# Optimization experiments

Measured on AMD Instinct MI355X. Metric: run time of the kernel, lower is better.

Reference implementation:

```python
import jax, jax.numpy as jnp
import numpy as np

MAX_SEGMENTS = 256
MAX_PIXELS = 400   # fixed-capacity bucket per segment
EMBED_DIM = 768
N_CHANNELS = 3


def setup_inputs() -> dict:
    key = jax.random.key(0)
    k1, k2, k3, k4 = jax.random.split(key, 4)
    img = jax.random.normal(k1, (32, N_CHANNELS, 384, 384), dtype=jnp.float32)
    segments = jax.random.randint(k2, (32, 384, 384), 0, MAX_SEGMENTS, dtype=jnp.int32)
    fan_in = N_CHANNELS * MAX_PIXELS
    proj_w = jax.random.normal(k3, (EMBED_DIM, fan_in), dtype=jnp.float32) / np.sqrt(fan_in).astype(np.float32)
    proj_b = jax.random.normal(k4, (EMBED_DIM,), dtype=jnp.float32) * 0.01
    return {"img": img, "segments": segments, "proj_w": proj_w, "proj_b": proj_b}


def _bucketize(img_flat, seg_flat):
    """img_flat: [C, N] pixels in row-major scan order; seg_flat: [N] int ids.
    Returns [S, C*P]: first P pixels (scan order) of each segment, zero padded,
    channel-major per segment — matching torch's masked gather + flatten."""
    C, N = img_flat.shape
    idx = jnp.arange(N, dtype=jnp.int32)
    # stable sort by segment id preserves scan order within each segment
    order = jnp.argsort(seg_flat, stable=True)
    sorted_seg = seg_flat[order]
    is_start = jnp.concatenate([jnp.ones((1,), bool), sorted_seg[1:] != sorted_seg[:-1]])
    group_start = jax.lax.cummax(jnp.where(is_start, idx, 0))
    rank_sorted = idx - group_start                      # position within segment
    rank = jnp.zeros((N,), jnp.int32).at[order].set(rank_sorted)
    dump = MAX_SEGMENTS * MAX_PIXELS                      # overflow slot (discarded)
    dest = jnp.where(rank < MAX_PIXELS, seg_flat.astype(jnp.int32) * MAX_PIXELS + rank, dump)
    buf = jnp.zeros((C, dump + 1), img_flat.dtype).at[:, dest].set(img_flat)
    # [C, S, P] -> [S, C, P] -> [S, C*P] (channel-major flatten per segment)
    return buf[:, :dump].reshape(C, MAX_SEGMENTS, MAX_PIXELS).transpose(1, 0, 2).reshape(MAX_SEGMENTS, C * MAX_PIXELS)


def reference(img, segments, proj_w, proj_b):
    B, C, H, W = img.shape
    feats = jax.vmap(_bucketize)(img.reshape(B, C, H * W), segments.reshape(B, H * W))
    # [B, S, C*P] @ [C*P, E] + [E]
    return feats @ proj_w.T + proj_b
```

## Files before the change

kernel.cpp:

```cpp
#include <hip/hip_runtime.h>
#include <hip/hip_bf16.h>
#include <cstdint>

#define BATCH 32
#define NCH 3
#define HW 147456
#define NSEG 256
#define NPIX 400
#define KDIM 1200
#define EDIM 768
#define MROWS (BATCH * NSEG)

#define CHUNK 4096
#define NCHUNK (HW / CHUNK)
#define NW 8
#define SUBW (CHUNK / NW)

#define ROW_BYTES 4800
#define APK_BYTES ((size_t)MROWS * ROW_BYTES)
#define W_BYTES (EDIM * KDIM * 4)

typedef __attribute__((ext_vector_type(8))) short short8b;
typedef __attribute__((ext_vector_type(16))) float f32x16;

__device__ __forceinline__ uint32_t bf16_rn(float f) {
    uint32_t u = __float_as_uint(f);
    return (u + 0x7fffu + ((u >> 16) & 1u)) >> 16;
}
__device__ __forceinline__ float bf16_tof(uint32_t h) { return __uint_as_float(h << 16); }
__device__ __forceinline__ uint32_t pack_split(float v) {
    uint32_t hi = bf16_rn(v);
    uint32_t lo = bf16_rn(v - bf16_tof(hi));
    return (lo << 16) | hi;
}

__device__ __forceinline__ void async_copy16(const void* gsrc, void* ldst) {
    __builtin_amdgcn_global_load_lds(
        (const __attribute__((address_space(1))) uint32_t*)gsrc,
        (__attribute__((address_space(3))) uint32_t*)ldst, 16, 0, 0);
}

__global__ __launch_bounds__(256) void hist_kernel(const int* __restrict__ seg,
                                                   int* __restrict__ cnt) {
    __shared__ int h[NSEG];
    const int tid = threadIdx.x;
    h[tid] = 0;
    __syncthreads();
    const int blk = blockIdx.x;
    const int b = blk / NCHUNK, ck = blk % NCHUNK;
    const int* segb = seg + (size_t)b * HW + ck * CHUNK;
#pragma unroll
    for (int i = 0; i < CHUNK / 256; ++i) atomicAdd(&h[segb[i * 256 + tid]], 1);
    __syncthreads();
    cnt[blk * NSEG + tid] = h[tid];
}

__global__ __launch_bounds__(256) void scan_kernel(int* __restrict__ cnt) {
    const int t = blockIdx.x * 256 + threadIdx.x;
    const int b = t >> 8, s = t & 255;
    int run = 0;
#pragma unroll
    for (int ck = 0; ck < NCHUNK; ++ck) {
        int* p = cnt + ((size_t)(b * NCHUNK + ck)) * NSEG + s;
        int v = *p;
        *p = run;
        run += v;
    }
    cnt[(size_t)(b * NCHUNK) * NSEG + s] = run;
}

__global__ __launch_bounds__(512) void scatter_kernel(const float* __restrict__ img,
                                                      const int* __restrict__ seg,
                                                      const int* __restrict__ base,
                                                      uint8_t* __restrict__ apk) {
    __shared__ int wpos[NW][NSEG];
    __shared__ int sl[NSEG];
    __shared__ uint32_t st0[CHUNK], st1[CHUNK], st2[CHUNK];

    const int tid = threadIdx.x;
    const int lane = tid & 63;
    const int wid = tid >> 6;
    const int blk = blockIdx.x;
    const int b = blk / NCHUNK, ck = blk % NCHUNK;

    int sb = 0;
    if (tid < NSEG) sb = (ck == 0) ? 0 : base[(size_t)blk * NSEG + tid];
#pragma unroll
    for (int i = 0; i < (NW * NSEG) / 512; ++i) ((int*)wpos)[i * 512 + tid] = 0;
    __syncthreads();

    const int* segb = seg + (size_t)b * HW;
    const float* imgb = img + (size_t)b * NCH * HW;
    const int startp = ck * CHUNK + wid * SUBW;
    const unsigned long long lt = (lane == 0) ? 0ull : ((~0ull) >> (64 - lane));

    int sv[SUBW / 64];
    unsigned long long mv[SUBW / 64];
#pragma unroll
    for (int g = 0; g < SUBW / 64; ++g) {
        const int p = startp + g * 64 + lane;
        const int s = segb[p];
        unsigned long long m = ~0ull;
#pragma unroll
        for (int bit = 0; bit < 8; ++bit) {
            unsigned long long bal = __ballot((s >> bit) & 1);
            m &= ((s >> bit) & 1) ? bal : ~bal;
        }
        sv[g] = s; mv[g] = m;
        if ((m & lt) == 0ull) atomicAdd(&wpos[wid][s], __popcll(m));
    }
    __syncthreads();

    int csum = 0;
    if (tid < NSEG) {
        int r = sb;
#pragma unroll
        for (int w = 0; w < NW; ++w) {
            const int t = wpos[w][tid];
            wpos[w][tid] = r;
            r += t;
        }
        csum = r - sb;
        sl[tid] = csum;
    }
    __syncthreads();
#pragma unroll
    for (int off = 1; off < NSEG; off <<= 1) {
        int y = 0;
        if (tid < NSEG && tid >= off) y = sl[tid - off];
        __syncthreads();
        if (tid < NSEG) sl[tid] += y;
        __syncthreads();
    }
    {
        int excl = 0;
        if (tid < NSEG) excl = sl[tid] - csum;
        __syncthreads();
        if (tid < NSEG) sl[tid] = (sb << 13) | excl;
    }
    __syncthreads();

#pragma unroll
    for (int g = 0; g < SUBW / 64; ++g) {
        const int p = startp + g * 64 + lane;
        const int s = sv[g];
        const unsigned long long m = mv[g];
        const int rig = __popcll(m & lt);
        const int leader = __ffsll((unsigned long long)m) - 1;
        int old = 0;
        if (rig == 0) old = atomicAdd(&wpos[wid][s], __popcll(m));
        old = __shfl(old, leader, 64);
        const int rank = old + rig;
        const int v = sl[s];
        const int j = rank - (v >> 13) + (v & 8191);
        st0[j] = pack_split(imgb[p]);
        st1[j] = pack_split(imgb[HW + p]);
        st2[j] = pack_split(imgb[2 * HW + p]);
    }
    __syncthreads();

    uint8_t* apkb = apk + (size_t)b * NSEG * ROW_BYTES;
#pragma unroll
    for (int it = 0; it < CHUNK / 512; ++it) {
        const int j = it * 512 + tid;
        int s = 0;
#pragma unroll
        for (int step = 128; step; step >>= 1) {
            const int c = s + step;
            if (c < NSEG && (sl[c] & 8191) <= j) s = c;
        }
        const int v = sl[s];
        const int rank = (v >> 13) + (j - (v & 8191));
        if (rank < NPIX) {
            uint16_t* hp = (uint16_t*)(apkb + (size_t)s * ROW_BYTES);
            uint16_t* lp = (uint16_t*)(apkb + (size_t)s * ROW_BYTES + 2400);
            const uint32_t v0 = st0[j], v1 = st1[j], v2 = st2[j];
            hp[rank]       = (uint16_t)v0;  lp[rank]       = (uint16_t)(v0 >> 16);
            hp[400 + rank] = (uint16_t)v1;  lp[400 + rank] = (uint16_t)(v1 >> 16);
            hp[800 + rank] = (uint16_t)v2;  lp[800 + rank] = (uint16_t)(v2 >> 16);
        }
    }
}

__global__ __launch_bounds__(256) void tailzero_kernel(uint8_t* __restrict__ apk,
                                                       const int* __restrict__ cnt) {
    const int tid = threadIdx.x;
    const int l = tid & 63;
    const int wid = tid >> 6;
    const int row = blockIdx.x * 4 + wid;
    const int b = row >> 8, s = row & 255;
    const int tot = cnt[(size_t)(b * NCHUNK) * NSEG + s];
    if (tot >= NPIX) return;
    uint16_t* hp = (uint16_t*)(apk + (size_t)row * ROW_BYTES);
    uint16_t* lp = (uint16_t*)(apk + (size_t)row * ROW_BYTES + 2400);
    for (int r = tot + l; r < NPIX; r += 64) {
        hp[r] = 0; lp[r] = 0;
        hp[400 + r] = 0; lp[400 + r] = 0;
        hp[800 + r] = 0; lp[800 + r] = 0;
    }
}

__global__ __launch_bounds__(256) void repackW_kernel(float* __restrict__ w) {
    __shared__ float buf[4][KDIM];
    const int tid = threadIdx.x;
    const int l = tid & 63;
    const int wid = tid >> 6;
    const int row = blockIdx.x * 4 + wid;
    float* rowp = w + (size_t)row * KDIM;
#pragma unroll
    for (int i = 0; i < 19; ++i) {
        const int idx = i * 64 + l;
        if (idx < KDIM) buf[wid][idx] = rowp[idx];
    }
    __syncthreads();
    uint32_t* rowu = (uint32_t*)rowp;
#pragma unroll
    for (int i = 0; i < 10; ++i) {
        const int j = i * 64 + l;
        if (j < KDIM / 2) {
            const float f0 = buf[wid][2 * j], f1 = buf[wid][2 * j + 1];
            const uint32_t h0 = bf16_rn(f0), h1 = bf16_rn(f1);
            const uint32_t l0 = bf16_rn(f0 - bf16_tof(h0));
            const uint32_t l1 = bf16_rn(f1 - bf16_tof(h1));
            rowu[j]            = h0 | (h1 << 16);
            rowu[KDIM / 2 + j] = l0 | (l1 << 16);
        }
    }
}

__global__ __launch_bounds__(256) void gemm_kernel(const uint8_t* __restrict__ A,
                                                   const uint8_t* __restrict__ Wp,
                                                   const float* __restrict__ bias,
                                                   float* __restrict__ out) {
    __shared__ uint8_t smem[49152];

    const int tid = threadIdx.x;
    const int l = tid & 63;
    const int wid = tid >> 6;
    const int wm = wid >> 1, wn = wid & 1;

    const int bid = blockIdx.x;
    const int xcd = bid & 7;
    const int t = bid >> 3;
    const int bn = t % 12;
    const int bm = (t / 12) * 8 + xcd;

    const int swzl = ((l & 7) * 16) ^ ((l >> 3) << 4);
    const int xread = (l & 7) << 4;

    const uint8_t* Abase = A + (size_t)bm * 128 * ROW_BYTES;

    f32x16 acc[2] = {};

    for (int k0 = 0; k0 < KDIM; k0 += 64) {
#pragma unroll
        for (int ii = 0; ii < 4; ++ii) {
            const int i = wid * 4 + ii;
            const int row = i * 8 + (l >> 3);
            const size_t gb = (size_t)row * ROW_BYTES + k0 * 2 + swzl;
            async_copy16(Abase + gb,        smem + i * 1024);
            async_copy16(Abase + gb + 2400, smem + 16384 + i * 1024);
        }
#pragma unroll
        for (int ii = 0; ii < 2; ++ii) {
            const int i = wid * 2 + ii;
            const int row = i * 8 + (l >> 3);
            const size_t gb = (size_t)(bn * 64 + row) * ROW_BYTES + k0 * 2 + swzl;
            async_copy16(Wp + gb, smem + 32768 + i * 1024);
            size_t gl = gb + 2400;
            if (gl + 16 > (size_t)W_BYTES) gl = 0;
            async_copy16(Wp + gl, smem + 40960 + i * 1024);
        }
        __syncthreads();

#pragma unroll
        for (int ks = 0; ks < 4; ++ks) {
            if (k0 + ks * 16 >= KDIM) break;
            const int koff = ks * 32 + ((l >> 5) * 16);
            short8b ahi[2], alo[2], bhi, blo;
#pragma unroll
            for (int mi = 0; mi < 2; ++mi) {
                const int row = wm * 64 + mi * 32 + (l & 31);
                const int byteA = row * 128 + (koff ^ xread);
                ahi[mi] = *(const short8b*)(smem + byteA);
                alo[mi] = *(const short8b*)(smem + 16384 + byteA);
            }
            {
                const int row = wn * 32 + (l & 31);
                const int byteB = row * 128 + (koff ^ xread);
                bhi = *(const short8b*)(smem + 32768 + byteB);
                blo = *(const short8b*)(smem + 40960 + byteB);
            }
#pragma unroll
            for (int mi = 0; mi < 2; ++mi) {
                acc[mi] = __builtin_amdgcn_mfma_f32_32x32x16_bf16(ahi[mi], bhi, acc[mi], 0, 0, 0);
                acc[mi] = __builtin_amdgcn_mfma_f32_32x32x16_bf16(ahi[mi], blo, acc[mi], 0, 0, 0);
                acc[mi] = __builtin_amdgcn_mfma_f32_32x32x16_bf16(alo[mi], bhi, acc[mi], 0, 0, 0);
            }
        }
        __syncthreads();
    }

    const int e = bn * 64 + wn * 32 + (l & 31);
    const float bv = bias[e];
#pragma unroll
    for (int mi = 0; mi < 2; ++mi) {
        const int rbase = bm * 128 + wm * 64 + mi * 32 + 4 * (l >> 5);
#pragma unroll
        for (int r = 0; r < 16; ++r) {
            const int row = rbase + (r & 3) + 8 * (r >> 2);
            out[(size_t)row * EDIM + e] = acc[mi][r] + bv;
        }
    }
}

extern "C" void kernel_launch(void* const* d_in, const int* in_sizes, int n_in,
                              void* d_out, int out_size, void* d_ws, size_t ws_size,
                              hipStream_t stream) {
    const float* img      = (const float*)d_in[0];
    const int*   segments = (const int*)d_in[1];
    float*       proj_w   = (float*)d_in[2];
    const float* proj_b   = (const float*)d_in[3];
    float* out = (float*)d_out;

    uint8_t* apk = (uint8_t*)d_ws;
    int*     cnt = (int*)((char*)d_ws + APK_BYTES);

    hist_kernel<<<BATCH * NCHUNK, 256, 0, stream>>>(segments, cnt);
    scan_kernel<<<MROWS / 256, 256, 0, stream>>>(cnt);
    repackW_kernel<<<EDIM / 4, 256, 0, stream>>>(proj_w);
    scatter_kernel<<<BATCH * NCHUNK, 512, 0, stream>>>(img, segments, cnt, apk);
    tailzero_kernel<<<MROWS / 4, 256, 0, stream>>>(apk, cnt);

    gemm_kernel<<<64 * 12, 256, 0, stream>>>(apk, (const uint8_t*)proj_w, proj_b, out);
}
```

Measured before the change: 224.8 us.

## Widen scatter blocks to 1024 threads, use wave-shuffle scan and segment map

```diff
diff --git a/kernel.cpp b/kernel.cpp
--- a/kernel.cpp
+++ b/kernel.cpp
@@ -13,7 +13,7 @@
 
 #define CHUNK 4096
 #define NCHUNK (HW / CHUNK)
-#define NW 8
+#define NW 16
 #define SUBW (CHUNK / NW)
 
 #define ROW_BYTES 4800
@@ -58,23 +58,26 @@
 __global__ __launch_bounds__(256) void scan_kernel(int* __restrict__ cnt) {
     const int t = blockIdx.x * 256 + threadIdx.x;
     const int b = t >> 8, s = t & 255;
+    int* basep = cnt + (size_t)(b * NCHUNK) * NSEG + s;
+    int v[NCHUNK];
+#pragma unroll
+    for (int ck = 0; ck < NCHUNK; ++ck) v[ck] = basep[ck * NSEG];
     int run = 0;
 #pragma unroll
-    for (int ck = 0; ck < NCHUNK; ++ck) {
-        int* p = cnt + ((size_t)(b * NCHUNK + ck)) * NSEG + s;
-        int v = *p;
-        *p = run;
-        run += v;
-    }
-    cnt[(size_t)(b * NCHUNK) * NSEG + s] = run;
-}
-
-__global__ __launch_bounds__(512) void scatter_kernel(const float* __restrict__ img,
-                                                      const int* __restrict__ seg,
-                                                      const int* __restrict__ base,
-                                                      uint8_t* __restrict__ apk) {
+    for (int ck = 0; ck < NCHUNK; ++ck) { const int x = v[ck]; v[ck] = run; run += x; }
+    v[0] = run;
+#pragma unroll
+    for (int ck = 0; ck < NCHUNK; ++ck) basep[ck * NSEG] = v[ck];
+}
+
+__global__ __launch_bounds__(1024) void scatter_kernel(const float* __restrict__ img,
+                                                       const int* __restrict__ seg,
+                                                       const int* __restrict__ base,
+                                                       uint8_t* __restrict__ apk) {
     __shared__ int wpos[NW][NSEG];
+    __shared__ int sbv[NSEG];
     __shared__ int sl[NSEG];
+    __shared__ uint8_t segmap[CHUNK];
     __shared__ uint32_t st0[CHUNK], st1[CHUNK], st2[CHUNK];
 
     const int tid = threadIdx.x;
@@ -83,10 +86,9 @@
     const int blk = blockIdx.x;
     const int b = blk / NCHUNK, ck = blk % NCHUNK;
 
-    int sb = 0;
-    if (tid < NSEG) sb = (ck == 0) ? 0 : base[(size_t)blk * NSEG + tid];
-#pragma unroll
-    for (int i = 0; i < (NW * NSEG) / 512; ++i) ((int*)wpos)[i * 512 + tid] = 0;
+    if (tid < NSEG) sbv[tid] = (ck == 0) ? 0 : base[(size_t)blk * NSEG + tid];
+#pragma unroll
+    for (int i = 0; i < (NW * NSEG) / 1024; ++i) ((int*)wpos)[i * 1024 + tid] = 0;
     __syncthreads();
 
     const int* segb = seg + (size_t)b * HW;
@@ -111,32 +113,32 @@
     }
     __syncthreads();
 
-    int csum = 0;
     if (tid < NSEG) {
-        int r = sb;
+        int r = sbv[tid];
 #pragma unroll
         for (int w = 0; w < NW; ++w) {
             const int t = wpos[w][tid];
             wpos[w][tid] = r;
             r += t;
         }
-        csum = r - sb;
-        sl[tid] = csum;
-    }
-    __syncthreads();
-#pragma unroll
-    for (int off = 1; off < NSEG; off <<= 1) {
-        int y = 0;
-        if (tid < NSEG && tid >= off) y = sl[tid - off];
-        __syncthreads();
-        if (tid < NSEG) sl[tid] += y;
-        __syncthreads();
-    }
-    {
-        int excl = 0;
-        if (tid < NSEG) excl = sl[tid] - csum;
-        __syncthreads();
-        if (tid < NSEG) sl[tid] = (sb << 13) | excl;
+        sl[tid] = r - sbv[tid];
+    }
+    __syncthreads();
+
+    if (wid == 0) {
+        int v0 = sl[lane * 4], v1 = sl[lane * 4 + 1], v2 = sl[lane * 4 + 2], v3 = sl[lane * 4 + 3];
+        const int mysum = v0 + v1 + v2 + v3;
+        int run = mysum;
+#pragma unroll
+        for (int off = 1; off < 64; off <<= 1) {
+            const int y = __shfl_up(run, off, 64);
+            if (lane >= off) run += y;
+        }
+        int e = run - mysum;
+        sl[lane * 4]     = (sbv[lane * 4]     << 13) | e;  e += v0;
+        sl[lane * 4 + 1] = (sbv[lane * 4 + 1] << 13) | e;  e += v1;
+        sl[lane * 4 + 2] = (sbv[lane * 4 + 2] << 13) | e;  e += v2;
+        sl[lane * 4 + 3] = (sbv[lane * 4 + 3] << 13) | e;
     }
     __syncthreads();
 
@@ -156,19 +158,15 @@
         st0[j] = pack_split(imgb[p]);
         st1[j] = pack_split(imgb[HW + p]);
         st2[j] = pack_split(imgb[2 * HW + p]);
+        segmap[j] = (uint8_t)s;
     }
     __syncthreads();
 
     uint8_t* apkb = apk + (size_t)b * NSEG * ROW_BYTES;
 #pragma unroll
-    for (int it = 0; it < CHUNK / 512; ++it) {
-        const int j = it * 512 + tid;
-        int s = 0;
-#pragma unroll
-        for (int step = 128; step; step >>= 1) {
-            const int c = s + step;
-            if (c < NSEG && (sl[c] & 8191) <= j) s = c;
-        }
+    for (int it = 0; it < CHUNK / 1024; ++it) {
+        const int j = it * 1024 + tid;
+        const int s = segmap[j];
         const int v = sl[s];
         const int rank = (v >> 13) + (j - (v & 8191));
         if (rank < NPIX) {
@@ -329,7 +327,7 @@
     hist_kernel<<<BATCH * NCHUNK, 256, 0, stream>>>(segments, cnt);
     scan_kernel<<<MROWS / 256, 256, 0, stream>>>(cnt);
     repackW_kernel<<<EDIM / 4, 256, 0, stream>>>(proj_w);
-    scatter_kernel<<<BATCH * NCHUNK, 512, 0, stream>>>(img, segments, cnt, apk);
+    scatter_kernel<<<BATCH * NCHUNK, 1024, 0, stream>>>(img, segments, cnt, apk);
     tailzero_kernel<<<MROWS / 4, 256, 0, stream>>>(apk, cnt);
 
     gemm_kernel<<<64 * 12, 256, 0, stream>>>(apk, (const uint8_t*)proj_w, proj_b, out);
```

Result: faster. 212.4 us (-5.5%).
